# Optimization experiments

Hardware: AMD Instinct MI355X
Metric: run time of the kernel (lower is better)

Reference implementation:

```python
import jax, jax.numpy as jnp
import numpy as np

HEADS = 8
DIM_HEAD = 64
SCALE = DIM_HEAD ** -0.5


def setup_inputs() -> dict:
    key = jax.random.key(0)
    ks = jax.random.split(key, 8)
    B, Nq, Nk, D = 4, 1024, 2048, 512
    inner = HEADS * DIM_HEAD  # 512
    x = jax.random.normal(ks[0], (B, Nq, D), dtype=jnp.float32)
    context = jax.random.normal(ks[1], (B, Nk, D), dtype=jnp.float32)
    bias = jax.random.normal(ks[2], (B, Nq, Nk), dtype=jnp.float32)
    s = D ** -0.5
    Wq = jax.random.normal(ks[3], (inner, D), dtype=jnp.float32) * s
    Wk = jax.random.normal(ks[4], (inner, D), dtype=jnp.float32) * s
    Wv = jax.random.normal(ks[5], (inner, D), dtype=jnp.float32) * s
    Wo = jax.random.normal(ks[6], (D, inner), dtype=jnp.float32) * s
    bo = jnp.zeros((D,), dtype=jnp.float32)
    return {"x": x, "context": context, "bias": bias,
            "Wq": Wq, "Wk": Wk, "Wv": Wv, "Wo": Wo, "bo": bo}


def reference(x, context, bias, Wq, Wk, Wv, Wo, bo):
    B, Nq, _ = x.shape
    # torch Linear: y = x @ W.T ; reshape (h d) -> b h n d
    q = (x @ Wq.T).reshape(B, Nq, HEADS, DIM_HEAD).transpose(0, 2, 1, 3)
    k = (context @ Wk.T).reshape(B, -1, HEADS, DIM_HEAD).transpose(0, 2, 1, 3)
    v = (context @ Wv.T).reshape(B, -1, HEADS, DIM_HEAD).transpose(0, 2, 1, 3)
    # explicit-score fallback path (bias supplied)
    scores = jnp.einsum('bhqd,bhkd->bhqk', q, k) * SCALE
    scores = scores + bias[:, None, :, :]  # 3D bias -> (B,1,Nq,Nk)
    attn = jax.nn.softmax(scores, axis=-1)
    out = jnp.einsum('bhqk,bhkd->bhqd', attn, v)
    out = out.transpose(0, 2, 1, 3).reshape(B, Nq, HEADS * DIM_HEAD)
    return out @ Wo.T + bo
```

## Files before the change

### kernel.cpp

```cpp
#include <hip/hip_runtime.h>

#define H 8
#define DH 64
#define NQ 1024
#define NK 2048
#define DIN 512
#define B 4
#define KSPLIT 2
#define KRANGE (NK / KSPLIT)
#define KTILES (KRANGE / 64)
#define BHNQ (B * H * NQ)

typedef __bf16 bf16;
typedef __bf16 bf16x8 __attribute__((ext_vector_type(8)));
typedef __bf16 bf16x4 __attribute__((ext_vector_type(4)));
typedef float floatx4 __attribute__((ext_vector_type(4)));

__device__ inline void gload16(const void* g, void* l) {
  __builtin_amdgcn_global_load_lds(
      (const __attribute__((address_space(1))) void*)g,
      (__attribute__((address_space(3))) void*)l, 16, 0, 0);
}

__global__ void cvt_all(const float* __restrict__ x, const float* __restrict__ ctx,
                        const float* __restrict__ wq, const float* __restrict__ wk,
                        const float* __restrict__ wv, const float* __restrict__ wo,
                        bf16* xb, bf16* cb, bf16* wqb, bf16* wkb, bf16* wvb, bf16* wob) {
  long i = ((long)blockIdx.x * 256 + threadIdx.x) * 4;
  const float* s; bf16* d; long o;
  if (i < 2097152)      { s = x;   d = xb;  o = i; }
  else if (i < 6291456) { s = ctx; d = cb;  o = i - 2097152; }
  else if (i < 6553600) { s = wq;  d = wqb; o = i - 6291456; }
  else if (i < 6815744) { s = wk;  d = wkb; o = i - 6553600; }
  else if (i < 7077888) { s = wv;  d = wvb; o = i - 6815744; }
  else                  { s = wo;  d = wob; o = i - 7077888; }
  float4 f = *(const float4*)(s + o);
  bf16x4 v = { (bf16)f.x, (bf16)f.y, (bf16)f.z, (bf16)f.w };
  *(bf16x4*)(d + o) = v;
}

__global__ __launch_bounds__(256) void gemm_qkv(
    const bf16* __restrict__ xb, const bf16* __restrict__ cb,
    const bf16* __restrict__ wqb, const bf16* __restrict__ wkb, const bf16* __restrict__ wvb,
    bf16* __restrict__ qb, bf16* __restrict__ kb, bf16* __restrict__ vtb) {
  const int which = blockIdx.z;
  if (which == 0 && blockIdx.y >= 64) return;
  const bf16* A = (which == 0) ? xb : cb;
  const bf16* W = (which == 0) ? wqb : ((which == 1) ? wkb : wvb);
  bf16* outb = (which == 0) ? qb : ((which == 1) ? kb : vtb);
  const int logT = (which == 0) ? 10 : 11;
  const float scale = (which == 0) ? 0.125f : 1.0f;
  const bool vmode = (which == 2);

  __shared__ bf16 Al[2][64 * 32];
  __shared__ bf16 Bl[2][128 * 32];
  const int t = threadIdx.x;
  const int lane = t & 63, w = t >> 6;
  const int ln = lane & 15, quad = lane >> 4;
  const int wm = (w >> 1) * 32, wn = (w & 1) * 64;
  const int rowBase = blockIdx.y * 64;
  const int colBase = blockIdx.x * 128;

  floatx4 acc[2][4] = {};
  const int rA = t >> 2, oA = (t & 3) * 8;
  const int c0 = t, c1 = t + 256;
  const int rB0 = c0 >> 2, oB0 = (c0 & 3) * 8;
  const int rB1 = c1 >> 2, oB1 = (c1 & 3) * 8;
  const bf16* Ab = A + (size_t)rowBase * DIN;
  const bf16* Wb = W + (size_t)colBase * DIN;

  gload16(Ab + (size_t)rA * DIN + oA, &Al[0][t * 8]);
  gload16(Wb + (size_t)rB0 * DIN + oB0, &Bl[0][c0 * 8]);
  gload16(Wb + (size_t)rB1 * DIN + oB1, &Bl[0][c1 * 8]);
  __syncthreads();

  for (int k0 = 0; k0 < DIN; k0 += 32) {
    const int cur = (k0 >> 5) & 1, nxt = cur ^ 1;
    if (k0 + 32 < DIN) {
      gload16(Ab + (size_t)rA * DIN + k0 + 32 + oA, &Al[nxt][t * 8]);
      gload16(Wb + (size_t)rB0 * DIN + k0 + 32 + oB0, &Bl[nxt][c0 * 8]);
      gload16(Wb + (size_t)rB1 * DIN + k0 + 32 + oB1, &Bl[nxt][c1 * 8]);
    }
    bf16x8 af[2], bfr[4];
#pragma unroll
    for (int i = 0; i < 2; i++)
      af[i] = *(const bf16x8*)&Al[cur][(wm + i * 16 + ln) * 32 + quad * 8];
#pragma unroll
    for (int j = 0; j < 4; j++)
      bfr[j] = *(const bf16x8*)&Bl[cur][(wn + j * 16 + ln) * 32 + quad * 8];
    if (!vmode) {
#pragma unroll
      for (int i = 0; i < 2; i++)
#pragma unroll
        for (int j = 0; j < 4; j++)
          acc[i][j] = __builtin_amdgcn_mfma_f32_16x16x32_bf16(af[i], bfr[j], acc[i][j], 0, 0, 0);
    } else {
#pragma unroll
      for (int i = 0; i < 2; i++)
#pragma unroll
        for (int j = 0; j < 4; j++)
          acc[i][j] = __builtin_amdgcn_mfma_f32_16x16x32_bf16(bfr[j], af[i], acc[i][j], 0, 0, 0);
    }
    __syncthreads();
  }

  const int T = 1 << logT;
#pragma unroll
  for (int i = 0; i < 2; i++)
#pragma unroll
    for (int j = 0; j < 4; j++)
#pragma unroll
      for (int r = 0; r < 4; r++) {
        if (!vmode) {
          const int m = rowBase + wm + i * 16 + quad * 4 + r;
          const int n = colBase + wn + j * 16 + ln;
          const float v = acc[i][j][r] * scale;
          const int bb = m >> logT, tok = m & (T - 1);
          const int hh = n >> 6, d = n & 63;
          outb[((((size_t)(bb * H + hh)) << logT) + tok) * DH + d] = (bf16)v;
        } else {
          const int dg = colBase + wn + j * 16 + quad * 4 + r;
          const int m = rowBase + wm + i * 16 + ln;
          const int bb = m >> logT, tok = m & (T - 1);
          const int hh = dg >> 6, d = dg & 63;
          outb[(((size_t)(bb * H + hh) * DH + d) << logT) + tok] = (bf16)acc[i][j][r];
        }
      }
}

__global__ __launch_bounds__(128) void attn_fwd(
    const bf16* __restrict__ q, const bf16* __restrict__ k,
    const bf16* __restrict__ vt, const float* __restrict__ bias,
    float* __restrict__ op0, float* __restrict__ op1, float* __restrict__ lpart) {
  __shared__ bf16 KL[64 * 64];
  __shared__ bf16 VL[64 * 64];
  __shared__ bf16 Pl[2][2][16 * 64];
  const int tid = threadIdx.x;
  const int lane = tid & 63, w = tid >> 6;
  const int ln = lane & 15, quad = lane >> 4;
  const int hh = blockIdx.y;
  const int b = blockIdx.z >> 1, ks = blockIdx.z & 1;
  const int q0 = blockIdx.x * 64;
  const int k0 = ks * KRANGE;
  const size_t bh = (size_t)b * H + hh;
  const bf16* qp = q + bh * NQ * DH;
  const bf16* kp = k + bh * NK * DH;
  const bf16* vp = vt + bh * DH * NK;
  const float* bp = bias + ((size_t)b * NQ + q0 + w * 32 + quad * 4) * NK + ln;

  bf16x8 qf[2][2];
#pragma unroll
  for (int s = 0; s < 2; s++)
#pragma unroll
    for (int kc = 0; kc < 2; kc++)
      qf[s][kc] = *(const bf16x8*)(qp + (size_t)(q0 + w * 32 + s * 16 + ln) * DH + kc * 32 + quad * 8);

  floatx4 o[2][4] = {};
  floatx4 lac[2] = {};
  const bf16x8 ones = {(bf16)1.f, (bf16)1.f, (bf16)1.f, (bf16)1.f,
                       (bf16)1.f, (bf16)1.f, (bf16)1.f, (bf16)1.f};
  constexpr float L2E = 1.44269504f;
  constexpr float OFF = 34.6246810f;

  for (int tt = 0; tt < KTILES; tt++) {
    const int nk0 = k0 + tt * 64;
#pragma unroll
    for (int s = 0; s < 4; s++) {
      const int i = s * 128 + tid;
      const int sr = i >> 3, sc = (i & 7) ^ (sr & 7);
      gload16(kp + (size_t)(nk0 + sr) * DH + sc * 8, &KL[i * 8]);
      gload16(vp + (size_t)sr * NK + nk0 + sc * 8, &VL[i * 8]);
    }
    float bc[2][4][4];
#pragma unroll
    for (int s = 0; s < 2; s++)
#pragma unroll
      for (int j = 0; j < 4; j++)
#pragma unroll
        for (int r = 0; r < 4; r++)
          bc[s][j][r] = bp[(size_t)(s * 16 + r) * NK + nk0 + j * 16];
    __syncthreads();

    floatx4 s4[2][4];
#pragma unroll
    for (int s = 0; s < 2; s++)
#pragma unroll
      for (int j = 0; j < 4; j++) {
        s4[s][j][0] = bc[s][j][0]; s4[s][j][1] = bc[s][j][1];
        s4[s][j][2] = bc[s][j][2]; s4[s][j][3] = bc[s][j][3];
      }
#pragma unroll
    for (int j = 0; j < 4; j++)
#pragma unroll
      for (int kc = 0; kc < 2; kc++) {
        const int kr = j * 16 + ln;
        bf16x8 kf = *(const bf16x8*)&KL[kr * 64 + (((kc * 4 + quad) ^ (kr & 7)) * 8)];
        s4[0][j] = __builtin_amdgcn_mfma_f32_16x16x32_bf16(qf[0][kc], kf, s4[0][j], 0, 0, 0);
        s4[1][j] = __builtin_amdgcn_mfma_f32_16x16x32_bf16(qf[1][kc], kf, s4[1][j], 0, 0, 0);
      }

#pragma unroll
    for (int s = 0; s < 2; s++)
#pragma unroll
      for (int j = 0; j < 4; j++)
#pragma unroll
        for (int r = 0; r < 4; r++)
          s4[s][j][r] = exp2f(fmaf(s4[s][j][r], L2E, -OFF));

#pragma unroll
    for (int s = 0; s < 2; s++)
#pragma unroll
      for (int j = 0; j < 4; j++)
#pragma unroll
        for (int r = 0; r < 4; r++) {
          const int m = quad * 4 + r;
          Pl[w][s][m * 64 + (((j * 2 + (ln >> 3)) ^ (m & 7)) * 8) + (ln & 7)] = (bf16)s4[s][j][r];
        }
    asm volatile("s_waitcnt lgkmcnt(0)" ::: "memory");
    bf16x8 pf[2][2];
#pragma unroll
    for (int s = 0; s < 2; s++)
#pragma unroll
      for (int kc = 0; kc < 2; kc++)
        pf[s][kc] = *(const bf16x8*)&Pl[w][s][ln * 64 + (((kc * 4 + quad) ^ (ln & 7)) * 8)];

#pragma unroll
    for (int s = 0; s < 2; s++)
#pragma unroll
      for (int kc = 0; kc < 2; kc++)
        lac[s] = __builtin_amdgcn_mfma_f32_16x16x32_bf16(pf[s][kc], ones, lac[s], 0, 0, 0);

#pragma unroll
    for (int jn = 0; jn < 4; jn++)
#pragma unroll
      for (int kc = 0; kc < 2; kc++) {
        const int vr = jn * 16 + ln;
        bf16x8 vf = *(const bf16x8*)&VL[vr * 64 + (((kc * 4 + quad) ^ (vr & 7)) * 8)];
        o[0][jn] = __builtin_amdgcn_mfma_f32_16x16x32_bf16(pf[0][kc], vf, o[0][jn], 0, 0, 0);
        o[1][jn] = __builtin_amdgcn_mfma_f32_16x16x32_bf16(pf[1][kc], vf, o[1][jn], 0, 0, 0);
      }
    __syncthreads();
  }

#pragma unroll
  for (int s = 0; s < 2; s++) {
    float* op = (ks ? op1 : op0) +
                ((size_t)b * NQ + q0 + w * 32 + s * 16 + quad * 4) * DIN + hh * 64 + ln;
#pragma unroll
    for (int jn = 0; jn < 4; jn++)
#pragma unroll
      for (int r = 0; r < 4; r++)
        op[(size_t)r * DIN + jn * 16] = o[s][jn][r];
    if (ln == 0) {
      float4 lv = {lac[s][0], lac[s][1], lac[s][2], lac[s][3]};
      *(float4*)&lpart[((size_t)ks * B * H + b * H + hh) * NQ + q0 + w * 32 + s * 16 + quad * 4] = lv;
    }
  }
}

__global__ __launch_bounds__(256) void gemm_out(
    const float* __restrict__ op0, const float* __restrict__ op1,
    const float* __restrict__ lp, const bf16* __restrict__ W,
    float* __restrict__ outf, const float* __restrict__ bo) {
  __shared__ bf16 Al[2][64 * 32];
  __shared__ bf16 Bl[2][128 * 32];
  const int t = threadIdx.x;
  const int lane = t & 63, w = t >> 6;
  const int ln = lane & 15, quad = lane >> 4;
  const int wm = (w >> 1) * 32, wn = (w & 1) * 64;
  const int rowBase = blockIdx.y * 64;
  const int colBase = blockIdx.x * 128;

  floatx4 acc[2][4] = {};
  const int rA = t >> 2, oA = (t & 3) * 8;
  const int c0 = t, c1 = t + 256;
  const int rB0 = c0 >> 2, oB0 = (c0 & 3) * 8;
  const int rB1 = c1 >> 2, oB1 = (c1 & 3) * 8;
  const int m0 = rowBase + rA;
  const bf16* Wb = W + (size_t)colBase * DIN;

  float linv0[8];
#pragma unroll
  for (int h = 0; h < 8; h++) {
    const int i0 = ((m0 >> 10) * H + h) * NQ + (m0 & 1023);
    linv0[h] = 1.0f / (lp[i0] + lp[BHNQ + i0]);
  }

#define STAGE_A(K0V, BUF)                                                      \
  {                                                                            \
    const float sA = linv0[(K0V) >> 6];                                        \
    const float* pa0 = op0 + (size_t)m0 * DIN + (K0V) + oA;                    \
    const float* pa1 = op1 + (size_t)m0 * DIN + (K0V) + oA;                    \
    float4 xa = *(const float4*)pa0, xb2 = *(const float4*)(pa0 + 4);          \
    float4 ya = *(const float4*)pa1, yb = *(const float4*)(pa1 + 4);           \
    bf16x8 v0 = {(bf16)((xa.x + ya.x) * sA), (bf16)((xa.y + ya.y) * sA),       \
                 (bf16)((xa.z + ya.z) * sA), (bf16)((xa.w + ya.w) * sA),       \
                 (bf16)((xb2.x + yb.x) * sA), (bf16)((xb2.y + yb.y) * sA),     \
                 (bf16)((xb2.z + yb.z) * sA), (bf16)((xb2.w + yb.w) * sA)};    \
    *(bf16x8*)&Al[BUF][t * 8] = v0;                                            \
  }

  STAGE_A(0, 0);
  gload16(Wb + (size_t)rB0 * DIN + oB0, &Bl[0][c0 * 8]);
  gload16(Wb + (size_t)rB1 * DIN + oB1, &Bl[0][c1 * 8]);
  __syncthreads();

#pragma unroll
  for (int kk = 0; kk < 16; kk++) {
    const int cur = kk & 1, nxt = cur ^ 1;
    if (kk < 15) {
      const int k1 = (kk + 1) * 32;
      STAGE_A(k1, nxt);
      gload16(Wb + (size_t)rB0 * DIN + k1 + oB0, &Bl[nxt][c0 * 8]);
      gload16(Wb + (size_t)rB1 * DIN + k1 + oB1, &Bl[nxt][c1 * 8]);
    }
    bf16x8 af[2], bfr[4];
#pragma unroll
    for (int i = 0; i < 2; i++)
      af[i] = *(const bf16x8*)&Al[cur][(wm + i * 16 + ln) * 32 + quad * 8];
#pragma unroll
    for (int j = 0; j < 4; j++)
      bfr[j] = *(const bf16x8*)&Bl[cur][(wn + j * 16 + ln) * 32 + quad * 8];
#pragma unroll
    for (int i = 0; i < 2; i++)
#pragma unroll
      for (int j = 0; j < 4; j++)
        acc[i][j] = __builtin_amdgcn_mfma_f32_16x16x32_bf16(af[i], bfr[j], acc[i][j], 0, 0, 0);
    __syncthreads();
  }
#undef STAGE_A

#pragma unroll
  for (int i = 0; i < 2; i++)
#pragma unroll
    for (int j = 0; j < 4; j++)
#pragma unroll
      for (int r = 0; r < 4; r++) {
        const int m = rowBase + wm + i * 16 + quad * 4 + r;
        const int n = colBase + wn + j * 16 + ln;
        outf[(size_t)m * DIN + n] = acc[i][j][r] + bo[n];
      }
}

extern "C" void kernel_launch(void* const* d_in, const int* in_sizes, int n_in,
                              void* d_out, int out_size, void* d_ws, size_t ws_size,
                              hipStream_t stream) {
  const float* x    = (const float*)d_in[0];
  const float* ctx  = (const float*)d_in[1];
  const float* bias = (const float*)d_in[2];
  const float* Wq   = (const float*)d_in[3];
  const float* Wk   = (const float*)d_in[4];
  const float* Wv   = (const float*)d_in[5];
  const float* Wo   = (const float*)d_in[6];
  const float* bo   = (const float*)d_in[7];
  float* out = (float*)d_out;

  char* p = (char*)d_ws;
  bf16* xb   = (bf16*)(p + 0);
  bf16* cb   = (bf16*)(p + 4194304);
  bf16* wqb  = (bf16*)(p + 12582912);
  bf16* wkb  = (bf16*)(p + 13107200);
  bf16* wvb  = (bf16*)(p + 13631488);
  bf16* wob  = (bf16*)(p + 14155776);
  bf16* qb   = (bf16*)(p + 14680064);
  bf16* kb   = (bf16*)(p + 18874368);
  bf16* vtb  = (bf16*)(p + 27262976);
  float* op1 = (float*)(p + 35651584);
  float* lpart = (float*)(p + 44040192);
  float* op0 = (float*)cb;

  cvt_all<<<7168, 256, 0, stream>>>(x, ctx, Wq, Wk, Wv, Wo, xb, cb, wqb, wkb, wvb, wob);
  gemm_qkv<<<dim3(4, 128, 3), 256, 0, stream>>>(xb, cb, wqb, wkb, wvb, qb, kb, vtb);
  attn_fwd<<<dim3(NQ / 64, H, B * KSPLIT), 128, 0, stream>>>(qb, kb, vtb, bias, op0, op1, lpart);
  gemm_out<<<dim3(4, 64), 256, 0, stream>>>(op0, op1, lpart, wob, out, bo);
}
```

Measured before the change: 196.7 us.

## Double-buffer K/V tiles and bias prefetch in attention kernel

```diff
diff --git a/kernel.cpp b/kernel.cpp
--- a/kernel.cpp
+++ b/kernel.cpp
@@ -132,8 +132,8 @@
     const bf16* __restrict__ q, const bf16* __restrict__ k,
     const bf16* __restrict__ vt, const float* __restrict__ bias,
     float* __restrict__ op0, float* __restrict__ op1, float* __restrict__ lpart) {
-  __shared__ bf16 KL[64 * 64];
-  __shared__ bf16 VL[64 * 64];
+  __shared__ bf16 KL[2][64 * 64];
+  __shared__ bf16 VL[2][64 * 64];
   __shared__ bf16 Pl[2][2][16 * 64];
   const int tid = threadIdx.x;
   const int lane = tid & 63, w = tid >> 6;
@@ -162,85 +162,114 @@
   constexpr float L2E = 1.44269504f;
   constexpr float OFF = 34.6246810f;
 
-  for (int tt = 0; tt < KTILES; tt++) {
-    const int nk0 = k0 + tt * 64;
-#pragma unroll
-    for (int s = 0; s < 4; s++) {
-      const int i = s * 128 + tid;
-      const int sr = i >> 3, sc = (i & 7) ^ (sr & 7);
-      gload16(kp + (size_t)(nk0 + sr) * DH + sc * 8, &KL[i * 8]);
-      gload16(vp + (size_t)sr * NK + nk0 + sc * 8, &VL[i * 8]);
+  float bcA[2][4][4], bcB[2][4][4];
+
+#define STAGE(NB, TT)                                                      \
+  {                                                                        \
+    const int nk0_ = k0 + (TT) * 64;                                       \
+    _Pragma("unroll")                                                      \
+    for (int s_ = 0; s_ < 4; s_++) {                                       \
+      const int i_ = s_ * 128 + tid;                                       \
+      const int sr_ = i_ >> 3, sc_ = (i_ & 7) ^ (sr_ & 7);                 \
+      gload16(kp + (size_t)(nk0_ + sr_) * DH + sc_ * 8, &KL[NB][i_ * 8]);  \
+      gload16(vp + (size_t)sr_ * NK + nk0_ + sc_ * 8, &VL[NB][i_ * 8]);    \
+    }                                                                      \
+  }
+
+#define LOADB(BC, TT)                                                      \
+  {                                                                        \
+    const int nk0_ = k0 + (TT) * 64;                                       \
+    _Pragma("unroll")                                                      \
+    for (int s_ = 0; s_ < 2; s_++)                                         \
+      _Pragma("unroll")                                                    \
+      for (int j_ = 0; j_ < 4; j_++)                                       \
+        _Pragma("unroll")                                                  \
+        for (int r_ = 0; r_ < 4; r_++)                                     \
+          BC[s_][j_][r_] = bp[(size_t)(s_ * 16 + r_) * NK + nk0_ + j_ * 16]; \
+  }
+
+#define COMPUTE(CUR, BC)                                                              \
+  {                                                                                   \
+     \
+    floatx4 s4[2][4];                                                                 \
+    _Pragma("unroll")                                                                 \
+    for (int s_ = 0; s_ < 2; s_++)                                                    \
+      _Pragma("unroll")                                                               \
+      for (int j_ = 0; j_ < 4; j_++) {                                                \
+        s4[s_][j_][0] = BC[s_][j_][0]; s4[s_][j_][1] = BC[s_][j_][1];                 \
+        s4[s_][j_][2] = BC[s_][j_][2]; s4[s_][j_][3] = BC[s_][j_][3];                 \
+      }                                                                               \
+    _Pragma("unroll")                                                                 \
+    for (int j_ = 0; j_ < 4; j_++)                                                    \
+      _Pragma("unroll")                                                               \
+      for (int kc_ = 0; kc_ < 2; kc_++) {                                             \
+        const int kr_ = j_ * 16 + ln;                                                 \
+        bf16x8 kf = *(const bf16x8*)&KL[CUR][kr_ * 64 + (((kc_ * 4 + quad) ^ (kr_ & 7)) * 8)]; \
+        s4[0][j_] = __builtin_amdgcn_mfma_f32_16x16x32_bf16(qf[0][kc_], kf, s4[0][j_], 0, 0, 0); \
+        s4[1][j_] = __builtin_amdgcn_mfma_f32_16x16x32_bf16(qf[1][kc_], kf, s4[1][j_], 0, 0, 0); \
+      }                                                                               \
+                                                 \
+    _Pragma("unroll")                                                                 \
+    for (int s_ = 0; s_ < 2; s_++)                                                    \
+      _Pragma("unroll")                                                               \
+      for (int j_ = 0; j_ < 4; j_++)                                                  \
+        _Pragma("unroll")                                                             \
+        for (int r_ = 0; r_ < 4; r_++)                                                \
+          s4[s_][j_][r_] = exp2f(fmaf(s4[s_][j_][r_], L2E, -OFF));                    \
+          \
+    _Pragma("unroll")                                                                 \
+    for (int s_ = 0; s_ < 2; s_++)                                                    \
+      _Pragma("unroll")                                                               \
+      for (int j_ = 0; j_ < 4; j_++)                                                  \
+        _Pragma("unroll")                                                             \
+        for (int r_ = 0; r_ < 4; r_++) {                                              \
+          const int m_ = quad * 4 + r_;                                               \
+          Pl[w][s_][m_ * 64 + (((j_ * 2 + (ln >> 3)) ^ (m_ & 7)) * 8) + (ln & 7)] = (bf16)s4[s_][j_][r_]; \
+        }                                                                             \
+    asm volatile("s_waitcnt lgkmcnt(0)" ::: "memory");                                \
+    bf16x8 pf[2][2];                                                                  \
+    _Pragma("unroll")                                                                 \
+    for (int s_ = 0; s_ < 2; s_++)                                                    \
+      _Pragma("unroll")                                                               \
+      for (int kc_ = 0; kc_ < 2; kc_++)                                               \
+        pf[s_][kc_] = *(const bf16x8*)&Pl[w][s_][ln * 64 + (((kc_ * 4 + quad) ^ (ln & 7)) * 8)]; \
+                                                         \
+    _Pragma("unroll")                                                                 \
+    for (int s_ = 0; s_ < 2; s_++)                                                    \
+      _Pragma("unroll")                                                               \
+      for (int kc_ = 0; kc_ < 2; kc_++)                                               \
+        lac[s_] = __builtin_amdgcn_mfma_f32_16x16x32_bf16(pf[s_][kc_], ones, lac[s_], 0, 0, 0); \
+                   \
+    _Pragma("unroll")                                                                 \
+    for (int jn_ = 0; jn_ < 4; jn_++)                                                 \
+      _Pragma("unroll")                                                               \
+      for (int kc_ = 0; kc_ < 2; kc_++) {                                             \
+        const int vr_ = jn_ * 16 + ln;                                                \
+        bf16x8 vf = *(const bf16x8*)&VL[CUR][vr_ * 64 + (((kc_ * 4 + quad) ^ (vr_ & 7)) * 8)]; \
+        o[0][jn_] = __builtin_amdgcn_mfma_f32_16x16x32_bf16(pf[0][kc_], vf, o[0][jn_], 0, 0, 0); \
+        o[1][jn_] = __builtin_amdgcn_mfma_f32_16x16x32_bf16(pf[1][kc_], vf, o[1][jn_], 0, 0, 0); \
+      }                                                                               \
+  }
+
+  STAGE(0, 0);
+  LOADB(bcA, 0);
+  __syncthreads();
+
+  for (int tt = 0; tt < KTILES; tt += 2) {
+    STAGE(1, tt + 1);
+    LOADB(bcB, tt + 1);
+    COMPUTE(0, bcA);
+    __syncthreads();
+    if (tt + 2 < KTILES) {
+      STAGE(0, tt + 2);
+      LOADB(bcA, tt + 2);
     }
-    float bc[2][4][4];
-#pragma unroll
-    for (int s = 0; s < 2; s++)
-#pragma unroll
-      for (int j = 0; j < 4; j++)
-#pragma unroll
-        for (int r = 0; r < 4; r++)
-          bc[s][j][r] = bp[(size_t)(s * 16 + r) * NK + nk0 + j * 16];
+    COMPUTE(1, bcB);
     __syncthreads();
-
-    floatx4 s4[2][4];
-#pragma unroll
-    for (int s = 0; s < 2; s++)
-#pragma unroll
-      for (int j = 0; j < 4; j++) {
-        s4[s][j][0] = bc[s][j][0]; s4[s][j][1] = bc[s][j][1];
-        s4[s][j][2] = bc[s][j][2]; s4[s][j][3] = bc[s][j][3];
-      }
-#pragma unroll
-    for (int j = 0; j < 4; j++)
-#pragma unroll
-      for (int kc = 0; kc < 2; kc++) {
-        const int kr = j * 16 + ln;
-        bf16x8 kf = *(const bf16x8*)&KL[kr * 64 + (((kc * 4 + quad) ^ (kr & 7)) * 8)];
-        s4[0][j] = __builtin_amdgcn_mfma_f32_16x16x32_bf16(qf[0][kc], kf, s4[0][j], 0, 0, 0);
-        s4[1][j] = __builtin_amdgcn_mfma_f32_16x16x32_bf16(qf[1][kc], kf, s4[1][j], 0, 0, 0);
-      }
-
-#pragma unroll
-    for (int s = 0; s < 2; s++)
-#pragma unroll
-      for (int j = 0; j < 4; j++)
-#pragma unroll
-        for (int r = 0; r < 4; r++)
-          s4[s][j][r] = exp2f(fmaf(s4[s][j][r], L2E, -OFF));
-
-#pragma unroll
-    for (int s = 0; s < 2; s++)
-#pragma unroll
-      for (int j = 0; j < 4; j++)
-#pragma unroll
-        for (int r = 0; r < 4; r++) {
-          const int m = quad * 4 + r;
-          Pl[w][s][m * 64 + (((j * 2 + (ln >> 3)) ^ (m & 7)) * 8) + (ln & 7)] = (bf16)s4[s][j][r];
-        }
-    asm volatile("s_waitcnt lgkmcnt(0)" ::: "memory");
-    bf16x8 pf[2][2];
-#pragma unroll
-    for (int s = 0; s < 2; s++)
-#pragma unroll
-      for (int kc = 0; kc < 2; kc++)
-        pf[s][kc] = *(const bf16x8*)&Pl[w][s][ln * 64 + (((kc * 4 + quad) ^ (ln & 7)) * 8)];
-
-#pragma unroll
-    for (int s = 0; s < 2; s++)
-#pragma unroll
-      for (int kc = 0; kc < 2; kc++)
-        lac[s] = __builtin_amdgcn_mfma_f32_16x16x32_bf16(pf[s][kc], ones, lac[s], 0, 0, 0);
-
-#pragma unroll
-    for (int jn = 0; jn < 4; jn++)
-#pragma unroll
-      for (int kc = 0; kc < 2; kc++) {
-        const int vr = jn * 16 + ln;
-        bf16x8 vf = *(const bf16x8*)&VL[vr * 64 + (((kc * 4 + quad) ^ (vr & 7)) * 8)];
-        o[0][jn] = __builtin_amdgcn_mfma_f32_16x16x32_bf16(pf[0][kc], vf, o[0][jn], 0, 0, 0);
-        o[1][jn] = __builtin_amdgcn_mfma_f32_16x16x32_bf16(pf[1][kc], vf, o[1][jn], 0, 0, 0);
-      }
-    __syncthreads();
-  }
+  }
+#undef STAGE
+#undef LOADB
+#undef COMPUTE
 
 #pragma unroll
   for (int s = 0; s < 2; s++) {
```

New measurement: 210.7 us. +7.1%, slower.
